# Optimization experiments

Measured on AMD Instinct MI355X. Metric: run time of the kernel, lower is better.

The kernel has to match this reference:

```python
import jax, jax.numpy as jnp
import numpy as np

B, T, D = 2, 2048, 1024
H, HS = 16, 64
EPS = 1e-5

def _ln(x, g, b):
    m = jnp.mean(x, axis=-1, keepdims=True)
    v = jnp.mean((x - m) ** 2, axis=-1, keepdims=True)
    return (x - m) * jax.lax.rsqrt(v + EPS) * g + b

def setup_inputs() -> dict:
    key = jax.random.key(0)
    ks = jax.random.split(key, 8)
    s_in = 1.0 / np.sqrt(D)
    s_ff = 1.0 / np.sqrt(4 * D)
    return {
        "embds": jax.random.normal(ks[0], (B, T, D), jnp.float32),
        "Wq": jax.random.normal(ks[1], (H, D, HS), jnp.float32) * s_in,
        "Wk": jax.random.normal(ks[2], (H, D, HS), jnp.float32) * s_in,
        "Wv": jax.random.normal(ks[3], (H, D, HS), jnp.float32) * s_in,
        "ln1_g": jnp.ones((D,), jnp.float32),
        "ln1_b": jnp.zeros((D,), jnp.float32),
        "ln2_g": jnp.ones((D,), jnp.float32),
        "ln2_b": jnp.zeros((D,), jnp.float32),
        "W1": jax.random.normal(ks[4], (D, 4 * D), jnp.float32) * s_in,
        "b1": jnp.zeros((4 * D,), jnp.float32),
        "W2": jax.random.normal(ks[5], (4 * D, D), jnp.float32) * s_ff,
        "b2": jnp.zeros((D,), jnp.float32),
    }

def reference(embds, Wq, Wk, Wv, ln1_g, ln1_b, ln2_g, ln2_b, W1, b1, W2, b2):
    _, t, d = embds.shape
    x = _ln(embds, ln1_g, ln1_b)
    q = jnp.einsum("btd,hde->bhte", x, Wq)
    k = jnp.einsum("btd,hde->bhte", x, Wk)
    v = jnp.einsum("btd,hde->bhte", x, Wv)
    # NOTE: repo scales by num_embds**-0.5 (C of input), not head_size**-0.5
    scores = jnp.einsum("bhte,bhse->bhts", q, k) * (d ** -0.5)
    causal = jnp.tril(jnp.ones((t, t), bool))
    scores = jnp.where(causal, scores, -jnp.inf)
    w = jax.nn.softmax(scores, axis=-1)
    o = jnp.einsum("bhts,bhse->bhte", w, v)  # [B,H,T,HS]
    attn = o.transpose(0, 2, 1, 3).reshape(embds.shape[0], t, -1)  # concat heads
    embds = embds + attn
    y = _ln(embds, ln2_g, ln2_b)
    ff = jax.nn.relu(y @ W1 + b1) @ W2 + b2
    return embds + ff
```

## Files before the change

kernel.cpp:

```cpp
#include <hip/hip_runtime.h>

using s16x8 = __attribute__((ext_vector_type(8))) short;
using f32x4 = __attribute__((ext_vector_type(4))) float;
typedef unsigned int   u32;
typedef unsigned short u16;

__device__ __forceinline__ u16 f2bf(float f) {
  u32 u = __float_as_uint(f);
  u += 0x7fffu + ((u >> 16) & 1u);
  return (u16)(u >> 16);
}
__device__ __forceinline__ float bf2f(u16 s) {
  return __uint_as_float(((u32)s) << 16);
}

typedef __attribute__((address_space(1))) const unsigned int g_u32;
typedef __attribute__((address_space(3))) unsigned int l_u32;
__device__ __forceinline__ void gload16(const void* g, void* l) {
  __builtin_amdgcn_global_load_lds((g_u32*)g, (l_u32*)l, 16, 0, 0);
}

__device__ __forceinline__ size_t kfrag_addr(int bh, int t, int e) {
  const int pair = (((t >> 4) & 3) << 1) + (e >> 5);
  const int slot = ((e >> 3) & 3) * 16 + (t & 15);
  return ((((size_t)bh * 32 + (t >> 6)) * 8 + pair) * 64 + slot) * 8 + (e & 7);
}
__device__ __forceinline__ size_t vfrag_addr(int bh, int t, int e) {
  const int pair = (((e >> 4) & 3) << 1) + ((t >> 5) & 1);
  const int slot = ((t >> 3) & 3) * 16 + (e & 15);
  return ((((size_t)bh * 32 + (t >> 6)) * 8 + pair) * 64 + slot) * 8 + (t & 7);
}

__global__ __launch_bounds__(256) void transpose_pack(
    const float* __restrict__ src, u16* __restrict__ dst, int R, int C)
{
  __shared__ u16 tile[64][66];
  const int tid = threadIdx.x;
  const int c0 = blockIdx.x * 64, r0 = blockIdx.y * 64;
  const size_t zoff = (size_t)blockIdx.z * R * C;
  src += zoff; dst += zoff;
  const int rr = tid >> 6, cc = tid & 63;
  #pragma unroll
  for (int i = 0; i < 16; ++i)
    tile[i * 4 + rr][cc] = f2bf(src[(size_t)(r0 + i * 4 + rr) * C + c0 + cc]);
  __syncthreads();
  #pragma unroll
  for (int i = 0; i < 16; ++i)
    dst[(size_t)(c0 + i * 4 + rr) * R + r0 + cc] = tile[cc][i * 4 + rr];
}

__global__ __launch_bounds__(256) void ln_kernel(
    const float* __restrict__ x, const float* __restrict__ g,
    const float* __restrict__ be, u16* __restrict__ out)
{
  const int row = blockIdx.x, tid = threadIdx.x;
  const int lane = tid & 63, wave = tid >> 6;
  const float4 v = ((const float4*)(x + (size_t)row * 1024))[tid];
  float s  = v.x + v.y + v.z + v.w;
  float sq = v.x * v.x + v.y * v.y + v.z * v.z + v.w * v.w;
  #pragma unroll
  for (int m = 1; m < 64; m <<= 1) { s += __shfl_xor(s, m); sq += __shfl_xor(sq, m); }
  __shared__ float rs[4], rq[4];
  if (lane == 0) { rs[wave] = s; rq[wave] = sq; }
  __syncthreads();
  s  = rs[0] + rs[1] + rs[2] + rs[3];
  sq = rq[0] + rq[1] + rq[2] + rq[3];
  const float mean = s * (1.0f / 1024.0f);
  const float var  = sq * (1.0f / 1024.0f) - mean * mean;
  const float rstd = rsqrtf(var + 1e-5f);
  const int c = tid * 4;
  const float4 gv = ((const float4*)g)[tid];
  const float4 bv = ((const float4*)be)[tid];
  ushort4 o;
  o.x = f2bf((v.x - mean) * rstd * gv.x + bv.x);
  o.y = f2bf((v.y - mean) * rstd * gv.y + bv.y);
  o.z = f2bf((v.z - mean) * rstd * gv.z + bv.z);
  o.w = f2bf((v.w - mean) * rstd * gv.w + bv.w);
  *(ushort4*)&out[(size_t)row * 1024 + c] = o;
}

template<int MODE, int MR>
__global__ __launch_bounds__(256) void gemm128(
    const u16* __restrict__ A, const u16* __restrict__ BT, int K,
    u16* __restrict__ o0q, u16* __restrict__ o0k, u16* __restrict__ o0v,
    u16* __restrict__ o1, const float* __restrict__ bias,
    float* __restrict__ o2, const float* __restrict__ resid)
{
  constexpr int BM = 64 * MR;
  __shared__ alignas(16) u16 As[2][BM * 32];
  __shared__ alignas(16) u16 Bs[2][128 * 32];
  const int tid = threadIdx.x, lane = tid & 63, wave = tid >> 6;
  const int wr = wave >> 1, wc = wave & 1;
  const int gx = gridDim.x;
  const int nwg = gx * gridDim.y;
  int lid = blockIdx.y * gx + blockIdx.x;
  lid = (lid & 7) * (nwg >> 3) + (lid >> 3);
  const int row0 = (lid / gx) * BM, col0 = (lid % gx) * 128;
  const int fr = lane & 15, g = lane >> 4;
  const int swz = (g ^ ((fr >> 1) & 3)) * 8;

  const int sr = wave * 16 + (lane >> 2);
  const int sc = ((lane & 3) ^ ((lane >> 3) & 3)) * 8;
  const u16* Ap0 = A  + (size_t)(row0 + sr) * K + sc;
  const u16* Ap1 = A  + (size_t)(row0 + 64 + sr) * K + sc;
  const u16* Bp0 = BT + (size_t)(col0 + sr) * K + sc;
  const u16* Bp1 = BT + (size_t)(col0 + 64 + sr) * K + sc;

  f32x4 acc[2 * MR][4] = {};

  auto stage = [&](int sel, int k0) {
    gload16(Ap0 + k0, &As[sel][wave * 512]);
    if constexpr (MR == 2) gload16(Ap1 + k0, &As[sel][(4 + wave) * 512]);
    gload16(Bp0 + k0, &Bs[sel][wave * 512]);
    gload16(Bp1 + k0, &Bs[sel][(4 + wave) * 512]);
  };

  stage(0, 0);
  __syncthreads();
  int cur = 0;
  for (int k0 = 0; k0 < K; k0 += 32) {
    if (k0 + 32 < K) stage(cur ^ 1, k0 + 32);
    s16x8 af[2 * MR], bfr[4];
    #pragma unroll
    for (int m = 0; m < 2 * MR; ++m)
      af[m] = *(const s16x8*)&As[cur][(wr * (32 * MR) + m * 16 + fr) * 32 + swz];
    #pragma unroll
    for (int n = 0; n < 4; ++n)
      bfr[n] = *(const s16x8*)&Bs[cur][(wc * 64 + n * 16 + fr) * 32 + swz];
    #pragma unroll
    for (int m = 0; m < 2 * MR; ++m)
      #pragma unroll
      for (int n = 0; n < 4; ++n)
        acc[m][n] = __builtin_amdgcn_mfma_f32_16x16x32_bf16(af[m], bfr[n], acc[m][n], 0, 0, 0);
    __syncthreads();
    cur ^= 1;
  }

  const float QSCALE = 0.03125f * 1.4426950408889634f;
  #pragma unroll
  for (int m = 0; m < 2 * MR; ++m) {
    const int rbase = row0 + wr * (32 * MR) + m * 16 + g * 4;
    #pragma unroll
    for (int n = 0; n < 4; ++n) {
      const int col = col0 + wc * 64 + n * 16 + fr;
      if constexpr (MODE == 0) {
        const int w = col >> 10, h = (col >> 6) & 15, e = col & 63;
        const int b = rbase >> 11, t0 = rbase & 2047;
        const int bh = b * 16 + h;
        if (w == 0) {
          #pragma unroll
          for (int j = 0; j < 4; ++j)
            o0q[((size_t)bh * 2048 + (t0 + j)) * 64 + e] = f2bf(acc[m][n][j] * QSCALE);
        } else if (w == 1) {
          #pragma unroll
          for (int j = 0; j < 4; ++j)
            o0k[kfrag_addr(bh, t0 + j, e)] = f2bf(acc[m][n][j]);
        } else {
          ushort4 pk;
          pk.x = f2bf(acc[m][n][0]); pk.y = f2bf(acc[m][n][1]);
          pk.z = f2bf(acc[m][n][2]); pk.w = f2bf(acc[m][n][3]);
          *(ushort4*)&o0v[vfrag_addr(bh, t0, e)] = pk;
        }
      } else if constexpr (MODE == 1) {
        const float bb = bias[col];
        #pragma unroll
        for (int j = 0; j < 4; ++j) {
          float v = fmaxf(acc[m][n][j] + bb, 0.0f);
          o1[(size_t)(rbase + j) * 4096 + col] = f2bf(v);
        }
      } else {
        const float bb = bias[col];
        #pragma unroll
        for (int j = 0; j < 4; ++j) {
          const size_t ix = (size_t)(rbase + j) * 1024 + col;
          o2[ix] = acc[m][n][j] + bb + resid[ix];
        }
      }
    }
  }
}

__global__ __launch_bounds__(256) void attn_mfma(
    const u16* __restrict__ q, const u16* __restrict__ kfragG,
    const u16* __restrict__ vfragG, const float* __restrict__ embds,
    float* __restrict__ e2)
{
  __shared__ alignas(16) u16 kbuf[2][4096];
  __shared__ alignas(16) u16 vbuf[2][4096];
  __shared__ alignas(16) u16 p_sm[4][16][72];
  const int tid = threadIdx.x, lane = tid & 63, wave = tid >> 6;
  const int bh = blockIdx.x & 31;
  const int qb = 31 - (blockIdx.x >> 5);
  const int q0 = qb * 64 + wave * 16;
  const int b = bh >> 4, h = bh & 15;
  const int fr = lane & 15, g = lane >> 4;

  const u16* qp = q + ((size_t)bh * 2048 + q0 + fr) * 64 + g * 8;
  const s16x8 qf0 = *(const s16x8*)(qp);
  const s16x8 qf1 = *(const s16x8*)(qp + 32);

  f32x4 o_acc[4] = {};
  float lacc[4] = {};

  const size_t fragbase = (size_t)bh * 131072;
  const int p0 = wave * 2, p1 = wave * 2 + 1;
  const int nch = qb + 1;

  auto stage_kv = [&](int sel, int c) {
    const size_t cb = fragbase + (size_t)c * 4096;
    gload16(kfragG + cb + p0 * 512 + lane * 8, &kbuf[sel][p0 * 512]);
    gload16(kfragG + cb + p1 * 512 + lane * 8, &kbuf[sel][p1 * 512]);
    gload16(vfragG + cb + p0 * 512 + lane * 8, &vbuf[sel][p0 * 512]);
    gload16(vfragG + cb + p1 * 512 + lane * 8, &vbuf[sel][p1 * 512]);
  };

  stage_kv(0, 0);
  __syncthreads();
  int cur = 0;

  for (int c = 0; c < nch; ++c) {
    if (c + 1 < nch) stage_kv(cur ^ 1, c + 1);
    const int s0 = c * 64;

    f32x4 sacc[4] = {};
    #pragma unroll
    for (int n = 0; n < 4; ++n) {
      const s16x8 kf0 = *(const s16x8*)&kbuf[cur][(n * 2 + 0) * 512 + lane * 8];
      const s16x8 kf1 = *(const s16x8*)&kbuf[cur][(n * 2 + 1) * 512 + lane * 8];
      sacc[n] = __builtin_amdgcn_mfma_f32_16x16x32_bf16(qf0, kf0, sacc[n], 0, 0, 0);
      sacc[n] = __builtin_amdgcn_mfma_f32_16x16x32_bf16(qf1, kf1, sacc[n], 0, 0, 0);
    }

    if (s0 + 63 > q0) {
      #pragma unroll
      for (int n = 0; n < 4; ++n) {
        const int s = s0 + n * 16 + fr;
        #pragma unroll
        for (int j = 0; j < 4; ++j)
          if (s > q0 + g * 4 + j) sacc[n][j] = -1e30f;
      }
    }

    float p[4][4];
    #pragma unroll
    for (int n = 0; n < 4; ++n)
      #pragma unroll
      for (int j = 0; j < 4; ++j) {
        p[n][j] = __builtin_amdgcn_exp2f(sacc[n][j]);
        lacc[j] += p[n][j];
      }

    #pragma unroll
    for (int n = 0; n < 4; ++n)
      #pragma unroll
      for (int j = 0; j < 4; ++j)
        p_sm[wave][g * 4 + j][n * 16 + fr] = f2bf(p[n][j]);

    const s16x8 pf0 = *(const s16x8*)&p_sm[wave][fr][g * 8];
    const s16x8 pf1 = *(const s16x8*)&p_sm[wave][fr][32 + g * 8];

    #pragma unroll
    for (int n = 0; n < 4; ++n) {
      const s16x8 vf0 = *(const s16x8*)&vbuf[cur][(n * 2 + 0) * 512 + lane * 8];
      const s16x8 vf1 = *(const s16x8*)&vbuf[cur][(n * 2 + 1) * 512 + lane * 8];
      o_acc[n] = __builtin_amdgcn_mfma_f32_16x16x32_bf16(pf0, vf0, o_acc[n], 0, 0, 0);
      o_acc[n] = __builtin_amdgcn_mfma_f32_16x16x32_bf16(pf1, vf1, o_acc[n], 0, 0, 0);
    }

    __syncthreads();
    cur ^= 1;
  }

  #pragma unroll
  for (int j = 0; j < 4; ++j) {
    #pragma unroll
    for (int mm = 1; mm < 16; mm <<= 1) lacc[j] += __shfl_xor(lacc[j], mm);
  }

  #pragma unroll
  for (int n = 0; n < 4; ++n) {
    #pragma unroll
    for (int j = 0; j < 4; ++j) {
      const int t = q0 + g * 4 + j;
      const size_t oi = ((size_t)b * 2048 + t) * 1024 + (size_t)h * 64 + n * 16 + fr;
      e2[oi] = embds[oi] + o_acc[n][j] / lacc[j];
    }
  }
}

extern "C" void kernel_launch(void* const* d_in, const int* in_sizes, int n_in,
                              void* d_out, int out_size, void* d_ws, size_t ws_size,
                              hipStream_t stream) {
  const float* embds = (const float*)d_in[0];
  const float* Wq    = (const float*)d_in[1];
  const float* Wk    = (const float*)d_in[2];
  const float* Wv    = (const float*)d_in[3];
  const float* ln1g  = (const float*)d_in[4];
  const float* ln1b  = (const float*)d_in[5];
  const float* ln2g  = (const float*)d_in[6];
  const float* ln2b  = (const float*)d_in[7];
  const float* W1    = (const float*)d_in[8];
  const float* b1    = (const float*)d_in[9];
  const float* W2    = (const float*)d_in[10];
  const float* b2    = (const float*)d_in[11];
  float* out = (float*)d_out;

  char* ws = (char*)d_ws;
  u16*   xln   = (u16*)(ws);
  u16*   wqkvT = (u16*)(ws + (8ull  << 20));
  u16*   qbuf  = (u16*)(ws + (14ull << 20));
  u16*   kfrag = (u16*)(ws + (22ull << 20));
  u16*   vfrag = (u16*)(ws + (30ull << 20));
  float* e2    = (float*)(ws + (38ull << 20));
  u16*   ybuf  = (u16*)(ws + (54ull << 20));
  u16*   w1T   = (u16*)(ws + (62ull << 20));
  u16*   w2T   = (u16*)(ws + (70ull << 20));
  u16*   hid   = (u16*)(ws + (78ull << 20));

  transpose_pack<<<dim3(1, 16, 16), 256, 0, stream>>>(Wq, wqkvT, 1024, 64);
  transpose_pack<<<dim3(1, 16, 16), 256, 0, stream>>>(Wk, wqkvT + (1u << 20), 1024, 64);
  transpose_pack<<<dim3(1, 16, 16), 256, 0, stream>>>(Wv, wqkvT + (2u << 20), 1024, 64);
  transpose_pack<<<dim3(64, 16, 1), 256, 0, stream>>>(W1, w1T, 1024, 4096);
  transpose_pack<<<dim3(16, 64, 1), 256, 0, stream>>>(W2, w2T, 4096, 1024);
  ln_kernel<<<4096, 256, 0, stream>>>(embds, ln1g, ln1b, xln);
  gemm128<0, 2><<<dim3(24, 32), 256, 0, stream>>>(xln, wqkvT, 1024,
      qbuf, kfrag, vfrag, nullptr, nullptr, nullptr, nullptr);
  attn_mfma<<<1024, 256, 0, stream>>>(qbuf, kfrag, vfrag, embds, e2);
  ln_kernel<<<4096, 256, 0, stream>>>(e2, ln2g, ln2b, ybuf);
  gemm128<1, 2><<<dim3(32, 32), 256, 0, stream>>>(ybuf, w1T, 1024,
      nullptr, nullptr, nullptr, hid, b1, nullptr, nullptr);
  gemm128<2, 1><<<dim3(8, 64), 256, 0, stream>>>(hid, w2T, 4096,
      nullptr, nullptr, nullptr, nullptr, b2, out, e2);
}
```

Baseline: 225.0 us.

## Triple-buffer GEMM and attention LDS pipelines with single vmcnt barrier, merge QKV transposes

Replaces the double-buffered LDS loop in the GEMM and attention kernels with a three-stage ring. Each step now waits on a partial vmcnt and hits one barrier, so two tiles stay in flight and the trailing __syncthreads is dropped. The three Wq/Wk/Wv transpose launches are also merged into one kernel. The extra buffer raises LDS use, which may lower occupancy, and the hand-counted vmcnt values must match the number of loads issued per stage.

Result: no change. 225.2 us (+0.1%).

```diff
diff --git a/kernel.cpp b/kernel.cpp
--- a/kernel.cpp
+++ b/kernel.cpp
@@ -19,6 +19,8 @@
 __device__ __forceinline__ void gload16(const void* g, void* l) {
   __builtin_amdgcn_global_load_lds((g_u32*)g, (l_u32*)l, 16, 0, 0);
 }
+
+#define WAITB(N) asm volatile("s_waitcnt vmcnt(" #N ")\ns_barrier" ::: "memory")
 
 __device__ __forceinline__ size_t kfrag_addr(int bh, int t, int e) {
   const int pair = (((t >> 4) & 3) << 1) + (e >> 5);
@@ -47,6 +49,26 @@
   #pragma unroll
   for (int i = 0; i < 16; ++i)
     dst[(size_t)(c0 + i * 4 + rr) * R + r0 + cc] = tile[cc][i * 4 + rr];
+}
+
+__global__ __launch_bounds__(256) void transpose_qkv(
+    const float* __restrict__ Wq, const float* __restrict__ Wk,
+    const float* __restrict__ Wv, u16* __restrict__ dst)
+{
+  __shared__ u16 tile[64][66];
+  const int tid = threadIdx.x;
+  const int sel = blockIdx.z >> 4, head = blockIdx.z & 15;
+  const int r0 = blockIdx.y * 64;
+  const float* src = ((sel == 0) ? Wq : (sel == 1) ? Wk : Wv) + (size_t)head * 65536;
+  u16* d = dst + ((size_t)sel << 20) + (size_t)head * 65536;
+  const int rr = tid >> 6, cc = tid & 63;
+  #pragma unroll
+  for (int i = 0; i < 16; ++i)
+    tile[i * 4 + rr][cc] = f2bf(src[(size_t)(r0 + i * 4 + rr) * 64 + cc]);
+  __syncthreads();
+  #pragma unroll
+  for (int i = 0; i < 16; ++i)
+    d[(size_t)(i * 4 + rr) * 1024 + r0 + cc] = tile[cc][i * 4 + rr];
 }
 
 __global__ __launch_bounds__(256) void ln_kernel(
@@ -87,8 +109,8 @@
     float* __restrict__ o2, const float* __restrict__ resid)
 {
   constexpr int BM = 64 * MR;
-  __shared__ alignas(16) u16 As[2][BM * 32];
-  __shared__ alignas(16) u16 Bs[2][128 * 32];
+  __shared__ alignas(16) u16 As[3][BM * 32];
+  __shared__ alignas(16) u16 Bs[3][128 * 32];
   const int tid = threadIdx.x, lane = tid & 63, wave = tid >> 6;
   const int wr = wave >> 1, wc = wave & 1;
   const int gx = gridDim.x;
@@ -114,27 +136,35 @@
     gload16(Bp0 + k0, &Bs[sel][wave * 512]);
     gload16(Bp1 + k0, &Bs[sel][(4 + wave) * 512]);
   };
-
-  stage(0, 0);
-  __syncthreads();
-  int cur = 0;
-  for (int k0 = 0; k0 < K; k0 += 32) {
-    if (k0 + 32 < K) stage(cur ^ 1, k0 + 32);
+  auto compute = [&](int sel) {
     s16x8 af[2 * MR], bfr[4];
     #pragma unroll
     for (int m = 0; m < 2 * MR; ++m)
-      af[m] = *(const s16x8*)&As[cur][(wr * (32 * MR) + m * 16 + fr) * 32 + swz];
+      af[m] = *(const s16x8*)&As[sel][(wr * (32 * MR) + m * 16 + fr) * 32 + swz];
     #pragma unroll
     for (int n = 0; n < 4; ++n)
-      bfr[n] = *(const s16x8*)&Bs[cur][(wc * 64 + n * 16 + fr) * 32 + swz];
+      bfr[n] = *(const s16x8*)&Bs[sel][(wc * 64 + n * 16 + fr) * 32 + swz];
     #pragma unroll
     for (int m = 0; m < 2 * MR; ++m)
       #pragma unroll
       for (int n = 0; n < 4; ++n)
         acc[m][n] = __builtin_amdgcn_mfma_f32_16x16x32_bf16(af[m], bfr[n], acc[m][n], 0, 0, 0);
-    __syncthreads();
-    cur ^= 1;
-  }
+  };
+
+  const int nsteps = K / 32;
+  stage(0, 0);
+  stage(1, 32);
+  int cur = 0;
+  for (int t = 0; t < nsteps - 1; ++t) {
+    if constexpr (MR == 2) WAITB(4); else WAITB(3);
+    const int nxt = (cur == 2) ? 0 : cur + 1;
+    const int nn  = (nxt == 2) ? 0 : nxt + 1;
+    if (t + 2 < nsteps) stage(nn, (t + 2) * 32);
+    compute(cur);
+    cur = nxt;
+  }
+  WAITB(0);
+  compute(cur);
 
   const float QSCALE = 0.03125f * 1.4426950408889634f;
   #pragma unroll
@@ -185,8 +215,8 @@
     const u16* __restrict__ vfragG, const float* __restrict__ embds,
     float* __restrict__ e2)
 {
-  __shared__ alignas(16) u16 kbuf[2][4096];
-  __shared__ alignas(16) u16 vbuf[2][4096];
+  __shared__ alignas(16) u16 kbuf[3][4096];
+  __shared__ alignas(16) u16 vbuf[3][4096];
   __shared__ alignas(16) u16 p_sm[4][16][72];
   const int tid = threadIdx.x, lane = tid & 63, wave = tid >> 6;
   const int bh = blockIdx.x & 31;
@@ -213,24 +243,15 @@
     gload16(vfragG + cb + p0 * 512 + lane * 8, &vbuf[sel][p0 * 512]);
     gload16(vfragG + cb + p1 * 512 + lane * 8, &vbuf[sel][p1 * 512]);
   };
-
-  stage_kv(0, 0);
-  __syncthreads();
-  int cur = 0;
-
-  for (int c = 0; c < nch; ++c) {
-    if (c + 1 < nch) stage_kv(cur ^ 1, c + 1);
-    const int s0 = c * 64;
-
+  auto compute = [&](int sel, int s0) {
     f32x4 sacc[4] = {};
     #pragma unroll
     for (int n = 0; n < 4; ++n) {
-      const s16x8 kf0 = *(const s16x8*)&kbuf[cur][(n * 2 + 0) * 512 + lane * 8];
-      const s16x8 kf1 = *(const s16x8*)&kbuf[cur][(n * 2 + 1) * 512 + lane * 8];
+      const s16x8 kf0 = *(const s16x8*)&kbuf[sel][(n * 2 + 0) * 512 + lane * 8];
+      const s16x8 kf1 = *(const s16x8*)&kbuf[sel][(n * 2 + 1) * 512 + lane * 8];
       sacc[n] = __builtin_amdgcn_mfma_f32_16x16x32_bf16(qf0, kf0, sacc[n], 0, 0, 0);
       sacc[n] = __builtin_amdgcn_mfma_f32_16x16x32_bf16(qf1, kf1, sacc[n], 0, 0, 0);
     }
-
     if (s0 + 63 > q0) {
       #pragma unroll
       for (int n = 0; n < 4; ++n) {
@@ -240,7 +261,6 @@
           if (s > q0 + g * 4 + j) sacc[n][j] = -1e30f;
       }
     }
-
     float p[4][4];
     #pragma unroll
     for (int n = 0; n < 4; ++n)
@@ -249,27 +269,35 @@
         p[n][j] = __builtin_amdgcn_exp2f(sacc[n][j]);
         lacc[j] += p[n][j];
       }
-
     #pragma unroll
     for (int n = 0; n < 4; ++n)
       #pragma unroll
       for (int j = 0; j < 4; ++j)
         p_sm[wave][g * 4 + j][n * 16 + fr] = f2bf(p[n][j]);
-
     const s16x8 pf0 = *(const s16x8*)&p_sm[wave][fr][g * 8];
     const s16x8 pf1 = *(const s16x8*)&p_sm[wave][fr][32 + g * 8];
-
     #pragma unroll
     for (int n = 0; n < 4; ++n) {
-      const s16x8 vf0 = *(const s16x8*)&vbuf[cur][(n * 2 + 0) * 512 + lane * 8];
-      const s16x8 vf1 = *(const s16x8*)&vbuf[cur][(n * 2 + 1) * 512 + lane * 8];
+      const s16x8 vf0 = *(const s16x8*)&vbuf[sel][(n * 2 + 0) * 512 + lane * 8];
+      const s16x8 vf1 = *(const s16x8*)&vbuf[sel][(n * 2 + 1) * 512 + lane * 8];
       o_acc[n] = __builtin_amdgcn_mfma_f32_16x16x32_bf16(pf0, vf0, o_acc[n], 0, 0, 0);
       o_acc[n] = __builtin_amdgcn_mfma_f32_16x16x32_bf16(pf1, vf1, o_acc[n], 0, 0, 0);
     }
-
-    __syncthreads();
-    cur ^= 1;
-  }
+  };
+
+  stage_kv(0, 0);
+  if (nch > 1) stage_kv(1, 1);
+  int cur = 0;
+  for (int t = 0; t < nch - 1; ++t) {
+    WAITB(4);
+    const int nxt = (cur == 2) ? 0 : cur + 1;
+    const int nn  = (nxt == 2) ? 0 : nxt + 1;
+    if (t + 2 < nch) stage_kv(nn, t + 2);
+    compute(cur, t * 64);
+    cur = nxt;
+  }
+  WAITB(0);
+  compute(cur, (nch - 1) * 64);
 
   #pragma unroll
   for (int j = 0; j < 4; ++j) {
@@ -317,9 +345,7 @@
   u16*   w2T   = (u16*)(ws + (70ull << 20));
   u16*   hid   = (u16*)(ws + (78ull << 20));
 
-  transpose_pack<<<dim3(1, 16, 16), 256, 0, stream>>>(Wq, wqkvT, 1024, 64);
-  transpose_pack<<<dim3(1, 16, 16), 256, 0, stream>>>(Wk, wqkvT + (1u << 20), 1024, 64);
-  transpose_pack<<<dim3(1, 16, 16), 256, 0, stream>>>(Wv, wqkvT + (2u << 20), 1024, 64);
+  transpose_qkv<<<dim3(1, 16, 48), 256, 0, stream>>>(Wq, Wk, Wv, wqkvT);
   transpose_pack<<<dim3(64, 16, 1), 256, 0, stream>>>(W1, w1T, 1024, 4096);
   transpose_pack<<<dim3(16, 64, 1), 256, 0, stream>>>(W2, w2T, 4096, 1024);
   ln_kernel<<<4096, 256, 0, stream>>>(embds, ln1g, ln1b, xln);
```
